# Optimization experiments

Hardware: AMD Instinct MI355X
Metric: run time of the kernel (lower is better)

## Reference

```python
import jax, jax.numpy as jnp
import numpy as np

N = 50000      # nodes
E = 800000     # edges
D = 128        # hidden_dim == out_dim
VOCAB = 50000  # in_size


def setup_inputs() -> dict:
    key = jax.random.key(0)
    ks = jax.random.split(key, 8)
    batch = jax.random.randint(ks[0], (N,), 0, VOCAB)
    src = jax.random.randint(ks[1], (E,), 0, N)
    dst = jax.random.randint(ks[2], (E,), 0, N)
    emb = jax.random.normal(ks[3], (VOCAB, D), dtype=jnp.float32) * 0.02
    s = 1.0 / np.sqrt(D)
    W1 = jax.random.normal(ks[4], (D, D), dtype=jnp.float32) * s
    W2 = jax.random.normal(ks[5], (D, D), dtype=jnp.float32) * s
    W3 = jax.random.normal(ks[6], (D, D), dtype=jnp.float32) * s
    b1 = jnp.zeros((D,), jnp.float32)
    b2 = jnp.zeros((D,), jnp.float32)
    b3 = jnp.zeros((D,), jnp.float32)
    return {"batch": batch, "src": src, "dst": dst, "emb": emb,
            "W1": W1, "b1": b1, "W2": W2, "b2": b2, "W3": W3, "b3": b3}


def reference(batch, src, dst, emb, W1, b1, W2, b2, W3, b3):
    # embedding lookup over node ids
    x = emb[batch]  # [N, D]
    ones = jnp.ones((E,), x.dtype)
    # DGL GraphConv norm='both': symmetric normalization, degrees clamped >= 1
    deg_out = jnp.clip(jax.ops.segment_sum(ones, src, num_segments=N), 1.0)
    deg_in = jnp.clip(jax.ops.segment_sum(ones, dst, num_segments=N), 1.0)
    norm_src = deg_out ** -0.5  # [N]
    norm_dst = deg_in ** -0.5   # [N]

    def gcn_layer(h, W, b):
        m = (h * norm_src[:, None])[src]                       # gather src messages [E, D]
        agg = jax.ops.segment_sum(m, dst, num_segments=N)      # SpMM aggregate [N, D]
        agg = agg * norm_dst[:, None]
        # dropout p=0.0 is identity; activation is ReLU
        return jax.nn.relu(agg @ W + b)

    x = gcn_layer(x, W1, b1)
    x = gcn_layer(x, W2, b2)
    x = gcn_layer(x, W3, b3)
    return x
```

## Files before the change

### kernel.cpp

```cpp
#include <hip/hip_runtime.h>
#include <math.h>

typedef float f4 __attribute__((ext_vector_type(4)));
typedef float f32x4 __attribute__((ext_vector_type(4)));
typedef short s8 __attribute__((ext_vector_type(8)));
typedef short s4 __attribute__((ext_vector_type(4)));

static constexpr int N = 50000;
static constexpr int E = 800000;
static constexpr int D = 128;
static constexpr int SCAN_NB = (N + 255) / 256;
static constexpr int MBLK = 64;
static constexpr int GRID_M = (N + MBLK - 1) / MBLK;
static constexpr int N_PAD = GRID_M * MBLK;
static constexpr int WT_PITCH = 136;

__device__ inline unsigned short f32_bf16_rne(float x) {
    unsigned u = __float_as_uint(x);
    return (unsigned short)((u + 0x7FFF + ((u >> 16) & 1)) >> 16);
}
__device__ inline float bf16_f32(unsigned short h) {
    return __uint_as_float((unsigned)h << 16);
}

__global__ void deg_kernel(const int* __restrict__ src, const int* __restrict__ dst,
                           int* __restrict__ deg_out, int* __restrict__ deg_in) {
    int e = blockIdx.x * 256 + threadIdx.x;
    if (e < E) {
        atomicAdd(&deg_out[src[e]], 1);
        atomicAdd(&deg_in[dst[e]], 1);
    }
}

__global__ void norm_kernel(const int* __restrict__ deg_out, const int* __restrict__ deg_in,
                            float* __restrict__ norm_src, float* __restrict__ norm_dst) {
    int i = blockIdx.x * 256 + threadIdx.x;
    if (i < N) {
        norm_src[i] = rsqrtf(fmaxf((float)deg_out[i], 1.0f));
        norm_dst[i] = rsqrtf(fmaxf((float)deg_in[i], 1.0f));
    }
}

__global__ __launch_bounds__(256) void scan_bsum_kernel(const int* __restrict__ deg,
                                                        int* __restrict__ bsums) {
    int i = blockIdx.x * 256 + threadIdx.x;
    int v = (i < N) ? deg[i] : 0;
#pragma unroll
    for (int off = 1; off < 64; off <<= 1) v += __shfl_xor(v, off, 64);
    __shared__ int ws[4];
    if ((threadIdx.x & 63) == 0) ws[threadIdx.x >> 6] = v;
    __syncthreads();
    if (threadIdx.x == 0) bsums[blockIdx.x] = ws[0] + ws[1] + ws[2] + ws[3];
}

__global__ __launch_bounds__(256) void scan_bsums_kernel(int* __restrict__ bsums) {
    __shared__ int s[256];
    int t = threadIdx.x;
    s[t] = (t < SCAN_NB) ? bsums[t] : 0;
    __syncthreads();
    for (int off = 1; off < 256; off <<= 1) {
        int v = (t >= off) ? s[t - off] : 0;
        __syncthreads();
        s[t] += v;
        __syncthreads();
    }
    if (t < SCAN_NB) bsums[t] = (t == 0) ? 0 : s[t - 1];
}

__global__ __launch_bounds__(256) void scan_final_kernel(const int* __restrict__ deg,
                                                         const int* __restrict__ bsums,
                                                         int* __restrict__ row_ptr) {
    __shared__ int s[256];
    int b = blockIdx.x, t = threadIdx.x;
    int i = b * 256 + t;
    s[t] = (i < N) ? deg[i] : 0;
    __syncthreads();
    for (int off = 1; off < 256; off <<= 1) {
        int v = (t >= off) ? s[t - off] : 0;
        __syncthreads();
        s[t] += v;
        __syncthreads();
    }
    if (i < N) row_ptr[i + 1] = s[t] + bsums[b];
    if (i == 0) row_ptr[0] = 0;
}

__global__ void fill_kernel(const int* __restrict__ src, const int* __restrict__ dst,
                            const int* __restrict__ row_ptr, int* __restrict__ cursor,
                            int* __restrict__ csr_src) {
    int e = blockIdx.x * 256 + threadIdx.x;
    if (e < E) {
        int d = dst[e];
        int pos = row_ptr[d] + atomicAdd(&cursor[d], 1);
        csr_src[pos] = src[e];
    }
}

__global__ void gather_kernel(const int* __restrict__ batch, const float* __restrict__ emb,
                              const float* __restrict__ norm_src, float* __restrict__ hs) {
    int gid = blockIdx.x * 256 + threadIdx.x;
    int i = gid >> 5;
    int c = (gid & 31) << 2;
    if (i < N) {
        float s = norm_src[i];
        f4 v = *(const f4*)(emb + (size_t)batch[i] * D + c);
        *(f4*)(hs + (size_t)i * D + c) = v * s;
    }
}

__global__ void agg_kernel(const int* __restrict__ row_ptr, const int* __restrict__ csr_src,
                           const float* __restrict__ hs,
                           short* __restrict__ agg_h, short* __restrict__ agg_l) {
    int gid = blockIdx.x * 256 + threadIdx.x;
    int node = gid >> 6;
    if (node >= N) return;
    int lane = threadIdx.x & 63;
    int grp = lane >> 5;
    int col = (lane & 31) << 2;
    int beg = row_ptr[node], end = row_ptr[node + 1];

    f4 a0 = (f4)0.0f, a1 = (f4)0.0f, a2 = (f4)0.0f, a3 = (f4)0.0f;
    f4 a4 = (f4)0.0f, a5 = (f4)0.0f, a6 = (f4)0.0f, a7 = (f4)0.0f;
    int e = beg + grp;
    for (; e + 14 < end; e += 16) {
        int s0 = csr_src[e];
        int s1 = csr_src[e + 2];
        int s2 = csr_src[e + 4];
        int s3 = csr_src[e + 6];
        int s4 = csr_src[e + 8];
        int s5 = csr_src[e + 10];
        int s6 = csr_src[e + 12];
        int s7 = csr_src[e + 14];
        a0 += *(const f4*)(hs + (size_t)s0 * D + col);
        a1 += *(const f4*)(hs + (size_t)s1 * D + col);
        a2 += *(const f4*)(hs + (size_t)s2 * D + col);
        a3 += *(const f4*)(hs + (size_t)s3 * D + col);
        a4 += *(const f4*)(hs + (size_t)s4 * D + col);
        a5 += *(const f4*)(hs + (size_t)s5 * D + col);
        a6 += *(const f4*)(hs + (size_t)s6 * D + col);
        a7 += *(const f4*)(hs + (size_t)s7 * D + col);
    }
    for (; e < end; e += 2)
        a0 += *(const f4*)(hs + (size_t)csr_src[e] * D + col);
    a0 += a1; a2 += a3; a4 += a5; a6 += a7;
    a0 += a2; a4 += a6;
    a0 += a4;

    f4 o;
#pragma unroll
    for (int j = 0; j < 4; ++j)
        o[j] = a0[j] + __shfl_xor(a0[j], 32, 64);
    if (grp == 0) {
        s4 oh, ol;
#pragma unroll
        for (int j = 0; j < 4; ++j) {
            unsigned short h = f32_bf16_rne(o[j]);
            oh[j] = (short)h;
            ol[j] = (short)f32_bf16_rne(o[j] - bf16_f32(h));
        }
        *(s4*)(agg_h + (size_t)node * D + col) = oh;
        *(s4*)(agg_l + (size_t)node * D + col) = ol;
    }
}

__global__ void wprep_kernel(const float* __restrict__ W1, const float* __restrict__ W2,
                             const float* __restrict__ W3, short* __restrict__ wt) {
    int idx = blockIdx.x * 256 + threadIdx.x;
    if (idx >= 3 * D * D) return;
    int l = idx >> 14;
    int e = idx & (D * D - 1);
    int n = e >> 7, k = e & 127;
    const float* W = (l == 0) ? W1 : ((l == 1) ? W2 : W3);
    float w = W[(size_t)k * D + n];
    unsigned short h = f32_bf16_rne(w);
    unsigned short lo = f32_bf16_rne(w - bf16_f32(h));
    wt[(size_t)l * 2 * D * D + (size_t)n * D + k] = (short)h;
    wt[(size_t)l * 2 * D * D + D * D + (size_t)n * D + k] = (short)lo;
}

__global__ __launch_bounds__(256, 2) void gemm_mfma_kernel(
    const short* __restrict__ Ah, const short* __restrict__ Al,
    const short* __restrict__ wth,
    const float* __restrict__ bias, const float* __restrict__ norm_dst,
    const float* __restrict__ post, float* __restrict__ out) {
    __shared__ short wt_h[D * WT_PITCH];
    __shared__ short wt_l[D * WT_PITCH];

    int tid = threadIdx.x;
    const short* gh = wth;
    const short* gl = wth + (size_t)D * D;

#pragma unroll
    for (int it = 0; it < 8; ++it) {
        int c = tid + it * 256;
        int n = c >> 4, kc = c & 15;
        *(s8*)(&wt_h[n * WT_PITCH + kc * 8]) = *(const s8*)(gh + (size_t)n * D + kc * 8);
        *(s8*)(&wt_l[n * WT_PITCH + kc * 8]) = *(const s8*)(gl + (size_t)n * D + kc * 8);
    }
    __syncthreads();

    int wv = tid >> 6;
    int lane = tid & 63;
    int lg = lane >> 4;
    int lr = lane & 15;

    int arow = blockIdx.x * 64 + wv * 16 + lr;
    const short* ahp = Ah + (size_t)arow * D;
    const short* alp = Al + (size_t)arow * D;

    f32x4 acc[8];
#pragma unroll
    for (int nt = 0; nt < 8; ++nt) acc[nt] = (f32x4)0.0f;

#pragma unroll
    for (int kt = 0; kt < 4; ++kt) {
        int ko = kt * 32 + lg * 8;
        s8 ah = *(const s8*)(ahp + ko);
        s8 al = *(const s8*)(alp + ko);
#pragma unroll
        for (int nt = 0; nt < 8; ++nt) {
            int bidx = (nt * 16 + lr) * WT_PITCH + ko;
            s8 bh = *(const s8*)(&wt_h[bidx]);
            s8 bl = *(const s8*)(&wt_l[bidx]);
            acc[nt] = __builtin_amdgcn_mfma_f32_16x16x32_bf16(ah, bh, acc[nt], 0, 0, 0);
            acc[nt] = __builtin_amdgcn_mfma_f32_16x16x32_bf16(al, bh, acc[nt], 0, 0, 0);
            acc[nt] = __builtin_amdgcn_mfma_f32_16x16x32_bf16(ah, bl, acc[nt], 0, 0, 0);
        }
    }

    int r0 = blockIdx.x * 64 + wv * 16 + lg * 4;
    float nd[4], ps[4];
#pragma unroll
    for (int i = 0; i < 4; ++i) {
        int gr = r0 + i;
        nd[i] = (gr < N) ? norm_dst[gr] : 0.0f;
        ps[i] = (gr < N) ? (post ? post[gr] : 1.0f) : 0.0f;
    }
#pragma unroll
    for (int nt = 0; nt < 8; ++nt) {
        int col = nt * 16 + lr;
        float bv = bias[col];
#pragma unroll
        for (int i = 0; i < 4; ++i) {
            int gr = r0 + i;
            if (gr < N) {
                float v = fmaxf(acc[nt][i] * nd[i] + bv, 0.0f) * ps[i];
                out[(size_t)gr * D + col] = v;
            }
        }
    }
}

extern "C" void kernel_launch(void* const* d_in, const int* in_sizes, int n_in,
                              void* d_out, int out_size, void* d_ws, size_t ws_size,
                              hipStream_t stream) {
    const int*   batch = (const int*)d_in[0];
    const int*   src   = (const int*)d_in[1];
    const int*   dst   = (const int*)d_in[2];
    const float* emb   = (const float*)d_in[3];
    const float* W1    = (const float*)d_in[4];
    const float* b1    = (const float*)d_in[5];
    const float* W2    = (const float*)d_in[6];
    const float* b2    = (const float*)d_in[7];
    const float* W3    = (const float*)d_in[8];
    const float* b3    = (const float*)d_in[9];
    float* out = (float*)d_out;

    float* norm_src = (float*)d_ws;
    float* norm_dst = norm_src + N;
    int*   row_ptr  = (int*)(norm_dst + N);
    int*   csr_src  = row_ptr + (N + 1);
    float* hs       = (float*)(csr_src + E) + 3;
    short* agg_h    = (short*)(hs + (size_t)N_PAD * D);
    short* agg_l    = agg_h + (size_t)N_PAD * D;
    short* wt       = agg_l + (size_t)N_PAD * D;
    int*   deg_out  = (int*)agg_h;
    int*   deg_in   = deg_out + N;
    int*   cursor   = deg_in + N;
    int*   bsums    = cursor + N;

    hipMemsetAsync(deg_out, 0, 3 * (size_t)N * sizeof(int), stream);
    deg_kernel<<<(E + 255) / 256, 256, 0, stream>>>(src, dst, deg_out, deg_in);
    norm_kernel<<<(N + 255) / 256, 256, 0, stream>>>(deg_out, deg_in, norm_src, norm_dst);
    scan_bsum_kernel<<<SCAN_NB, 256, 0, stream>>>(deg_in, bsums);
    scan_bsums_kernel<<<1, 256, 0, stream>>>(bsums);
    scan_final_kernel<<<SCAN_NB, 256, 0, stream>>>(deg_in, bsums, row_ptr);
    fill_kernel<<<(E + 255) / 256, 256, 0, stream>>>(src, dst, row_ptr, cursor, csr_src);
    gather_kernel<<<((size_t)N * 32 + 255) / 256, 256, 0, stream>>>(batch, emb, norm_src, hs);
    wprep_kernel<<<(3 * D * D + 255) / 256, 256, 0, stream>>>(W1, W2, W3, wt);

    const float* bs[3] = {b1, b2, b3};
    for (int l = 0; l < 3; ++l) {
        bool last = (l == 2);
        agg_kernel<<<((size_t)N * 64 + 255) / 256, 256, 0, stream>>>(
            row_ptr, csr_src, hs, agg_h, agg_l);
        gemm_mfma_kernel<<<GRID_M, 256, 0, stream>>>(
            agg_h, agg_l, wt + (size_t)l * 2 * D * D, bs[l], norm_dst,
            last ? nullptr : norm_src,
            last ? out : hs);
    }
}
```

Before: 398.2 us.

## Fuse SpMM aggregation into MFMA GEMM layer kernel with ping-pong buffers

Merges the per-layer aggregation and GEMM kernels into one layer kernel. Each lane gathers its node's neighbor rows directly into registers in the MFMA A-fragment layout, splits the sums into bf16 hi/lo on the fly, then runs the split-bf16 MFMA against the weights held in shared memory. This removes the agg_h/agg_l round trip through global memory and three launches, and hs now alternates between two buffers. It also fuses the norm and block-sum scan kernels. The cost is a gather pattern of only one node per lane with 8 scattered 16B loads per edge, so memory-level parallelism and coalescing are much worse than the old wave-per-node gather, and load is uneven across lanes when degrees differ.

```diff
diff --git a/kernel.cpp b/kernel.cpp
--- a/kernel.cpp
+++ b/kernel.cpp
@@ -4,13 +4,12 @@
 typedef float f4 __attribute__((ext_vector_type(4)));
 typedef float f32x4 __attribute__((ext_vector_type(4)));
 typedef short s8 __attribute__((ext_vector_type(8)));
-typedef short s4 __attribute__((ext_vector_type(4)));
 
 static constexpr int N = 50000;
 static constexpr int E = 800000;
 static constexpr int D = 128;
 static constexpr int SCAN_NB = (N + 255) / 256;
-static constexpr int MBLK = 64;
+static constexpr int MBLK = 128;
 static constexpr int GRID_M = (N + MBLK - 1) / MBLK;
 static constexpr int N_PAD = GRID_M * MBLK;
 static constexpr int WT_PITCH = 136;
@@ -32,19 +31,17 @@
     }
 }
 
-__global__ void norm_kernel(const int* __restrict__ deg_out, const int* __restrict__ deg_in,
-                            float* __restrict__ norm_src, float* __restrict__ norm_dst) {
+__global__ __launch_bounds__(256) void scan_bsum_norm_kernel(
+    const int* __restrict__ deg_out, const int* __restrict__ deg_in,
+    float* __restrict__ norm_src, float* __restrict__ norm_dst,
+    int* __restrict__ bsums) {
     int i = blockIdx.x * 256 + threadIdx.x;
+    int v = 0;
     if (i < N) {
         norm_src[i] = rsqrtf(fmaxf((float)deg_out[i], 1.0f));
         norm_dst[i] = rsqrtf(fmaxf((float)deg_in[i], 1.0f));
-    }
-}
-
-__global__ __launch_bounds__(256) void scan_bsum_kernel(const int* __restrict__ deg,
-                                                        int* __restrict__ bsums) {
-    int i = blockIdx.x * 256 + threadIdx.x;
-    int v = (i < N) ? deg[i] : 0;
+        v = deg_in[i];
+    }
 #pragma unroll
     for (int off = 1; off < 64; off <<= 1) v += __shfl_xor(v, off, 64);
     __shared__ int ws[4];
@@ -105,61 +102,6 @@
         float s = norm_src[i];
         f4 v = *(const f4*)(emb + (size_t)batch[i] * D + c);
         *(f4*)(hs + (size_t)i * D + c) = v * s;
-    }
-}
-
-__global__ void agg_kernel(const int* __restrict__ row_ptr, const int* __restrict__ csr_src,
-                           const float* __restrict__ hs,
-                           short* __restrict__ agg_h, short* __restrict__ agg_l) {
-    int gid = blockIdx.x * 256 + threadIdx.x;
-    int node = gid >> 6;
-    if (node >= N) return;
-    int lane = threadIdx.x & 63;
-    int grp = lane >> 5;
-    int col = (lane & 31) << 2;
-    int beg = row_ptr[node], end = row_ptr[node + 1];
-
-    f4 a0 = (f4)0.0f, a1 = (f4)0.0f, a2 = (f4)0.0f, a3 = (f4)0.0f;
-    f4 a4 = (f4)0.0f, a5 = (f4)0.0f, a6 = (f4)0.0f, a7 = (f4)0.0f;
-    int e = beg + grp;
-    for (; e + 14 < end; e += 16) {
-        int s0 = csr_src[e];
-        int s1 = csr_src[e + 2];
-        int s2 = csr_src[e + 4];
-        int s3 = csr_src[e + 6];
-        int s4 = csr_src[e + 8];
-        int s5 = csr_src[e + 10];
-        int s6 = csr_src[e + 12];
-        int s7 = csr_src[e + 14];
-        a0 += *(const f4*)(hs + (size_t)s0 * D + col);
-        a1 += *(const f4*)(hs + (size_t)s1 * D + col);
-        a2 += *(const f4*)(hs + (size_t)s2 * D + col);
-        a3 += *(const f4*)(hs + (size_t)s3 * D + col);
-        a4 += *(const f4*)(hs + (size_t)s4 * D + col);
-        a5 += *(const f4*)(hs + (size_t)s5 * D + col);
-        a6 += *(const f4*)(hs + (size_t)s6 * D + col);
-        a7 += *(const f4*)(hs + (size_t)s7 * D + col);
-    }
-    for (; e < end; e += 2)
-        a0 += *(const f4*)(hs + (size_t)csr_src[e] * D + col);
-    a0 += a1; a2 += a3; a4 += a5; a6 += a7;
-    a0 += a2; a4 += a6;
-    a0 += a4;
-
-    f4 o;
-#pragma unroll
-    for (int j = 0; j < 4; ++j)
-        o[j] = a0[j] + __shfl_xor(a0[j], 32, 64);
-    if (grp == 0) {
-        s4 oh, ol;
-#pragma unroll
-        for (int j = 0; j < 4; ++j) {
-            unsigned short h = f32_bf16_rne(o[j]);
-            oh[j] = (short)h;
-            ol[j] = (short)f32_bf16_rne(o[j] - bf16_f32(h));
-        }
-        *(s4*)(agg_h + (size_t)node * D + col) = oh;
-        *(s4*)(agg_l + (size_t)node * D + col) = ol;
     }
 }
 
@@ -178,9 +120,9 @@
     wt[(size_t)l * 2 * D * D + D * D + (size_t)n * D + k] = (short)lo;
 }
 
-__global__ __launch_bounds__(256, 2) void gemm_mfma_kernel(
-    const short* __restrict__ Ah, const short* __restrict__ Al,
-    const short* __restrict__ wth,
+__global__ __launch_bounds__(512, 4) void layer_kernel(
+    const int* __restrict__ row_ptr, const int* __restrict__ csr_src,
+    const float* __restrict__ hs_in, const short* __restrict__ wth,
     const float* __restrict__ bias, const float* __restrict__ norm_dst,
     const float* __restrict__ post, float* __restrict__ out) {
     __shared__ short wt_h[D * WT_PITCH];
@@ -189,24 +131,78 @@
     int tid = threadIdx.x;
     const short* gh = wth;
     const short* gl = wth + (size_t)D * D;
-
-#pragma unroll
-    for (int it = 0; it < 8; ++it) {
-        int c = tid + it * 256;
+#pragma unroll
+    for (int it = 0; it < 4; ++it) {
+        int c = tid + it * 512;
         int n = c >> 4, kc = c & 15;
         *(s8*)(&wt_h[n * WT_PITCH + kc * 8]) = *(const s8*)(gh + (size_t)n * D + kc * 8);
         *(s8*)(&wt_l[n * WT_PITCH + kc * 8]) = *(const s8*)(gl + (size_t)n * D + kc * 8);
     }
-    __syncthreads();
 
     int wv = tid >> 6;
     int lane = tid & 63;
     int lg = lane >> 4;
     int lr = lane & 15;
-
-    int arow = blockIdx.x * 64 + wv * 16 + lr;
-    const short* ahp = Ah + (size_t)arow * D;
-    const short* alp = Al + (size_t)arow * D;
+    int node = blockIdx.x * MBLK + wv * 16 + lr;
+    int cbase = lg * 8;
+
+    f4 ga[8];
+#pragma unroll
+    for (int j = 0; j < 8; ++j) ga[j] = (f4)0.0f;
+
+    if (node < N) {
+        int beg = row_ptr[node], end = row_ptr[node + 1];
+        int e = beg;
+        for (; e + 1 < end; e += 2) {
+            const float* p0 = hs_in + (size_t)csr_src[e] * D + cbase;
+            const float* p1 = hs_in + (size_t)csr_src[e + 1] * D + cbase;
+            f4 v0 = *(const f4*)(p0);
+            f4 v1 = *(const f4*)(p0 + 4);
+            f4 v2 = *(const f4*)(p0 + 32);
+            f4 v3 = *(const f4*)(p0 + 36);
+            f4 v4 = *(const f4*)(p0 + 64);
+            f4 v5 = *(const f4*)(p0 + 68);
+            f4 v6 = *(const f4*)(p0 + 96);
+            f4 v7 = *(const f4*)(p0 + 100);
+            f4 u0 = *(const f4*)(p1);
+            f4 u1 = *(const f4*)(p1 + 4);
+            f4 u2 = *(const f4*)(p1 + 32);
+            f4 u3 = *(const f4*)(p1 + 36);
+            f4 u4 = *(const f4*)(p1 + 64);
+            f4 u5 = *(const f4*)(p1 + 68);
+            f4 u6 = *(const f4*)(p1 + 96);
+            f4 u7 = *(const f4*)(p1 + 100);
+            ga[0] += v0; ga[1] += v1; ga[2] += v2; ga[3] += v3;
+            ga[4] += v4; ga[5] += v5; ga[6] += v6; ga[7] += v7;
+            ga[0] += u0; ga[1] += u1; ga[2] += u2; ga[3] += u3;
+            ga[4] += u4; ga[5] += u5; ga[6] += u6; ga[7] += u7;
+        }
+        if (e < end) {
+            const float* p0 = hs_in + (size_t)csr_src[e] * D + cbase;
+            ga[0] += *(const f4*)(p0);
+            ga[1] += *(const f4*)(p0 + 4);
+            ga[2] += *(const f4*)(p0 + 32);
+            ga[3] += *(const f4*)(p0 + 36);
+            ga[4] += *(const f4*)(p0 + 64);
+            ga[5] += *(const f4*)(p0 + 68);
+            ga[6] += *(const f4*)(p0 + 96);
+            ga[7] += *(const f4*)(p0 + 100);
+        }
+    }
+
+    s8 ah[4], al[4];
+#pragma unroll
+    for (int kt = 0; kt < 4; ++kt) {
+#pragma unroll
+        for (int i = 0; i < 8; ++i) {
+            float x = (i < 4) ? ga[2 * kt][i] : ga[2 * kt + 1][i - 4];
+            unsigned short h = f32_bf16_rne(x);
+            ah[kt][i] = (short)h;
+            al[kt][i] = (short)f32_bf16_rne(x - bf16_f32(h));
+        }
+    }
+
+    __syncthreads();
 
     f32x4 acc[8];
 #pragma unroll
@@ -214,21 +210,19 @@
 
 #pragma unroll
     for (int kt = 0; kt < 4; ++kt) {
-        int ko = kt * 32 + lg * 8;
-        s8 ah = *(const s8*)(ahp + ko);
-        s8 al = *(const s8*)(alp + ko);
+        int ko = kt * 32 + cbase;
 #pragma unroll
         for (int nt = 0; nt < 8; ++nt) {
             int bidx = (nt * 16 + lr) * WT_PITCH + ko;
             s8 bh = *(const s8*)(&wt_h[bidx]);
             s8 bl = *(const s8*)(&wt_l[bidx]);
-            acc[nt] = __builtin_amdgcn_mfma_f32_16x16x32_bf16(ah, bh, acc[nt], 0, 0, 0);
-            acc[nt] = __builtin_amdgcn_mfma_f32_16x16x32_bf16(al, bh, acc[nt], 0, 0, 0);
-            acc[nt] = __builtin_amdgcn_mfma_f32_16x16x32_bf16(ah, bl, acc[nt], 0, 0, 0);
-        }
-    }
-
-    int r0 = blockIdx.x * 64 + wv * 16 + lg * 4;
+            acc[nt] = __builtin_amdgcn_mfma_f32_16x16x32_bf16(ah[kt], bh, acc[nt], 0, 0, 0);
+            acc[nt] = __builtin_amdgcn_mfma_f32_16x16x32_bf16(al[kt], bh, acc[nt], 0, 0, 0);
+            acc[nt] = __builtin_amdgcn_mfma_f32_16x16x32_bf16(ah[kt], bl, acc[nt], 0, 0, 0);
+        }
+    }
+
+    int r0 = blockIdx.x * MBLK + wv * 16 + lg * 4;
     float nd[4], ps[4];
 #pragma unroll
     for (int i = 0; i < 4; ++i) {
@@ -270,33 +264,33 @@
     float* norm_dst = norm_src + N;
     int*   row_ptr  = (int*)(norm_dst + N);
     int*   csr_src  = row_ptr + (N + 1);
-    float* hs       = (float*)(csr_src + E) + 3;
-    short* agg_h    = (short*)(hs + (size_t)N_PAD * D);
-    short* agg_l    = agg_h + (size_t)N_PAD * D;
-    short* wt       = agg_l + (size_t)N_PAD * D;
-    int*   deg_out  = (int*)agg_h;
+    float* hs_a     = (float*)(csr_src + E) + 3;
+    float* hs_b     = hs_a + (size_t)N_PAD * D;
+    short* wt       = (short*)(hs_b + (size_t)N_PAD * D);
+    int*   deg_out  = (int*)hs_a;
     int*   deg_in   = deg_out + N;
     int*   cursor   = deg_in + N;
     int*   bsums    = cursor + N;
 
     hipMemsetAsync(deg_out, 0, 3 * (size_t)N * sizeof(int), stream);
     deg_kernel<<<(E + 255) / 256, 256, 0, stream>>>(src, dst, deg_out, deg_in);
-    norm_kernel<<<(N + 255) / 256, 256, 0, stream>>>(deg_out, deg_in, norm_src, norm_dst);
-    scan_bsum_kernel<<<SCAN_NB, 256, 0, stream>>>(deg_in, bsums);
+    scan_bsum_norm_kernel<<<SCAN_NB, 256, 0, stream>>>(deg_out, deg_in,
+                                                       norm_src, norm_dst, bsums);
     scan_bsums_kernel<<<1, 256, 0, stream>>>(bsums);
     scan_final_kernel<<<SCAN_NB, 256, 0, stream>>>(deg_in, bsums, row_ptr);
-    fill_kernel<<<(E + 255) / 256, 256, 0, stream>>>(src, dst, row_ptr, cursor, csr_src);
-    gather_kernel<<<((size_t)N * 32 + 255) / 256, 256, 0, stream>>>(batch, emb, norm_src, hs);
+    fill_kernel<<<(E + 255) / 256, 256, 0, stream>>>(src, dst, row_ptr, cursor,
+                                                     csr_src);
+    gather_kernel<<<((size_t)N * 32 + 255) / 256, 256, 0, stream>>>(batch, emb,
+                                                                    norm_src, hs_a);
     wprep_kernel<<<(3 * D * D + 255) / 256, 256, 0, stream>>>(W1, W2, W3, wt);
 
     const float* bs[3] = {b1, b2, b3};
-    for (int l = 0; l < 3; ++l) {
-        bool last = (l == 2);
-        agg_kernel<<<((size_t)N * 64 + 255) / 256, 256, 0, stream>>>(
-            row_ptr, csr_src, hs, agg_h, agg_l);
-        gemm_mfma_kernel<<<GRID_M, 256, 0, stream>>>(
-            agg_h, agg_l, wt + (size_t)l * 2 * D * D, bs[l], norm_dst,
-            last ? nullptr : norm_src,
-            last ? out : hs);
-    }
-}
+    layer_kernel<<<GRID_M, 512, 0, stream>>>(row_ptr, csr_src, hs_a, wt,
+                                             bs[0], norm_dst, norm_src, hs_b);
+    layer_kernel<<<GRID_M, 512, 0, stream>>>(row_ptr, csr_src, hs_b,
+                                             wt + (size_t)2 * D * D,
+                                             bs[1], norm_dst, norm_src, hs_a);
+    layer_kernel<<<GRID_M, 512, 0, stream>>>(row_ptr, csr_src, hs_a,
+                                             wt + (size_t)4 * D * D,
+                                             bs[2], norm_dst, nullptr, out);
+}
```

Result: no change. 398.4 us (+0.0%).
